# Kernel optimization log

Hardware: AMD Instinct MI355X
Metric: run time of the kernel (lower is better)

## Reference

```python
import jax, jax.numpy as jnp
import numpy as np

B, C, H, W = 16, 3, 384, 1280
EPS = 1e-7


def setup_inputs() -> dict:
    key = jax.random.key(0)
    k1, k2, k3, k4 = jax.random.split(key, 4)
    source_image = jax.random.normal(k1, (B, C, H, W), jnp.float32)
    depth_map = jax.random.uniform(k2, (B, 1, H, W), jnp.float32, minval=0.1, maxval=80.0)
    pose = 0.05 * jax.random.normal(k3, (B, 6), jnp.float32)
    # realistic KITTI-style pinhole intrinsics, per-batch mild perturbation
    base = jnp.array([[0.58 * W, 0.0, 0.5 * W],
                      [0.0, 1.92 * H, 0.5 * H],
                      [0.0, 0.0, 1.0]], jnp.float32)
    noise = 1.0 + 0.01 * jax.random.normal(k4, (B, 3, 3), jnp.float32)
    intrinsic = base[None] * noise  # zero entries stay zero -> invertible
    return {"source_image": source_image, "depth_map": depth_map,
            "pose": pose, "intrinsic": intrinsic}


def rot_from_axisangle(aa):
    # aa: [B,3] -> [B,3,3] (Rodrigues)
    theta = jnp.linalg.norm(aa, axis=-1, keepdims=True)  # [B,1]
    axis = aa / (theta + EPS)
    c = jnp.cos(theta)
    s = jnp.sin(theta)
    t = 1.0 - c
    x, y, z = axis[:, 0:1], axis[:, 1:2], axis[:, 2:3]
    row0 = jnp.concatenate([t * x * x + c, t * x * y - s * z, t * z * x + s * y], axis=1)
    row1 = jnp.concatenate([t * x * y + s * z, t * y * y + c, t * y * z - s * x], axis=1)
    row2 = jnp.concatenate([t * z * x - s * y, t * y * z + s * x, t * z * z + c], axis=1)
    return jnp.stack([row0, row1, row2], axis=1)  # [B,3,3]


def bilinear_grid_sample(img, gx, gy):
    # img: [B,C,H,W]; gx,gy: [B,H,W] in [-1,1]; align_corners=True, padding zeros
    Bc, Cc, Hc, Wc = img.shape
    x = (gx + 1.0) * 0.5 * (Wc - 1)
    y = (gy + 1.0) * 0.5 * (Hc - 1)
    x0 = jnp.floor(x)
    y0 = jnp.floor(y)
    x1 = x0 + 1.0
    y1 = y0 + 1.0
    wx1 = x - x0
    wx0 = 1.0 - wx1
    wy1 = y - y0
    wy0 = 1.0 - wy1
    imgf = img.reshape(Bc, Cc, Hc * Wc)

    def gather(xi, yi):
        inb = ((xi >= 0) & (xi <= Wc - 1) & (yi >= 0) & (yi <= Hc - 1)).astype(img.dtype)
        xc = jnp.clip(xi, 0, Wc - 1).astype(jnp.int32)
        yc = jnp.clip(yi, 0, Hc - 1).astype(jnp.int32)
        idx = (yc * Wc + xc).reshape(Bc, 1, -1)
        vals = jnp.take_along_axis(imgf, jnp.broadcast_to(idx, (Bc, Cc, idx.shape[-1])), axis=2)
        return vals.reshape(Bc, Cc, Hc, Wc) * inb[:, None]

    out = (gather(x0, y0) * (wx0 * wy0)[:, None]
           + gather(x1, y0) * (wx1 * wy0)[:, None]
           + gather(x0, y1) * (wx0 * wy1)[:, None]
           + gather(x1, y1) * (wx1 * wy1)[:, None])
    return out


def reference(source_image, depth_map, pose, intrinsic):
    Bb, _, Hh, Ww = depth_map.shape
    # pixel grid, homogeneous [H,W,3] = (x, y, 1)
    ys, xs = jnp.meshgrid(jnp.arange(Hh, dtype=depth_map.dtype),
                          jnp.arange(Ww, dtype=depth_map.dtype), indexing='ij')
    pix = jnp.stack([xs, ys, jnp.ones_like(xs)], axis=-1)  # [H,W,3]
    # backproject: K^{-1} @ pix * depth
    inv_K = jnp.linalg.inv(intrinsic)  # [B,3,3]
    cam = jnp.einsum('bij,hwj->bhwi', inv_K, pix)  # [B,H,W,3]
    frustum = cam * jnp.transpose(depth_map, (0, 2, 3, 1))  # [B,H,W,3]
    # rigid transform
    R = rot_from_axisangle(pose[:, :3])  # [B,3,3]
    t = pose[:, 3:]  # [B,3]
    points = jnp.einsum('bij,bhwj->bhwi', R, frustum) + t[:, None, None, :]
    # project with K
    coord = jnp.einsum('bij,bhwj->bhwi', intrinsic, points)  # [B,H,W,3]
    z = coord[..., 2] + EPS
    px = coord[..., 0] / z
    py = coord[..., 1] / z
    gx = px / (Ww - 1) * 2.0 - 1.0
    gy = py / (Hh - 1) * 2.0 - 1.0
    return bilinear_grid_sample(source_image, gx, gy)
```

## Files before the change

### kernel.cpp

```cpp
#include <hip/hip_runtime.h>
#include <hip/hip_fp16.h>

#define B_ 16
#define C_ 3
#define H_ 384
#define W_ 1280
#define HW_ (H_*W_)
#define EPS_ 1e-7f

#define NXCD_ 8

#define BANDS_ (W_/256)
#define RTILES_ (H_/2)
#define NBLK3_ (BANDS_*RTILES_*B_)
#define CPX3_  (NBLK3_/NXCD_)

typedef float v2f __attribute__((ext_vector_type(2)));
typedef float v4f __attribute__((ext_vector_type(4)));

__device__ __forceinline__ v2f load2(const float* p) {
  v2f r; __builtin_memcpy(&r, p, 8); return r;
}
__device__ __forceinline__ uint4 load16u(const void* p) {
  uint4 r; __builtin_memcpy(&r, p, 16); return r;
}
__device__ __forceinline__ v4f ntload4(const float* p) {
  return __builtin_nontemporal_load((const v4f*)p);
}
__device__ __forceinline__ void storent2(float* p, float a, float b) {
  v2f r; r.x = a; r.y = b;
  __builtin_nontemporal_store(r, (v2f*)p);
}
__device__ __forceinline__ unsigned pack2(float a, float b) {
  __half2 h = __floats2half2_rn(a, b);
  unsigned u; __builtin_memcpy(&u, &h, 4); return u;
}

__device__ __forceinline__ void mat3mul(const float* A, const float* Bm, float* C) {
  #pragma unroll
  for (int i = 0; i < 3; i++)
    #pragma unroll
    for (int j = 0; j < 3; j++)
      C[i*3+j] = A[i*3+0]*Bm[0*3+j] + A[i*3+1]*Bm[1*3+j] + A[i*3+2]*Bm[2*3+j];
}

__device__ void compute_MT(const float* __restrict__ pose,
                           const float* __restrict__ intr,
                           int b, float* M, float* T)
{
  float K[9];
  #pragma unroll
  for (int i = 0; i < 9; i++) K[i] = intr[b*9 + i];
  float aa0 = pose[b*6 + 0], aa1 = pose[b*6 + 1], aa2 = pose[b*6 + 2];
  float t0  = pose[b*6 + 3], t1  = pose[b*6 + 4], t2  = pose[b*6 + 5];

  float theta = sqrtf(aa0*aa0 + aa1*aa1 + aa2*aa2);
  float invn  = 1.0f / (theta + EPS_);
  float x = aa0*invn, y = aa1*invn, z = aa2*invn;
  float c = cosf(theta), s = sinf(theta), t = 1.0f - c;
  float R[9] = {
    t*x*x + c,   t*x*y - s*z, t*z*x + s*y,
    t*x*y + s*z, t*y*y + c,   t*y*z - s*x,
    t*z*x - s*y, t*y*z + s*x, t*z*z + c
  };

  float a = K[0], bb = K[1], cc = K[2];
  float d = K[3], e  = K[4], f  = K[5];
  float g = K[6], h  = K[7], ii = K[8];
  float A0 = e*ii - f*h, A1 = f*g - d*ii, A2 = d*h - e*g;
  float id = 1.0f / (a*A0 + bb*A1 + cc*A2);
  float iK[9] = {
    A0*id, (cc*h - bb*ii)*id, (bb*f - cc*e)*id,
    A1*id, (a*ii - cc*g)*id,  (cc*d - a*f)*id,
    A2*id, (bb*g - a*h)*id,   (a*e  - bb*d)*id
  };

  float KR[9];
  mat3mul(K, R, KR);
  mat3mul(KR, iK, M);
  T[0] = K[0]*t0 + K[1]*t1 + K[2]*t2;
  T[1] = K[3]*t0 + K[4]*t1 + K[5]*t2;
  T[2] = K[6]*t0 + K[7]*t1 + K[8]*t2;
}

__global__ __launch_bounds__(256) void repack_kernel(
    const float* __restrict__ src, uint4* __restrict__ ws)
{
  int tg = blockIdx.x * 256 + threadIdx.x;
  int b  = tg / (HW_/4);
  int p  = (tg - b * (HW_/4)) * 4;
  const float* s = src + (size_t)b * 3 * HW_ + p;
  v4f c0 = ntload4(s);
  v4f c1 = ntload4(s + HW_);
  v4f c2 = ntload4(s + 2*HW_);
  uint4 o0, o1;
  o0.x = pack2(c0.x, c1.x); o0.y = pack2(c2.x, 0.0f);
  o0.z = pack2(c0.y, c1.y); o0.w = pack2(c2.y, 0.0f);
  o1.x = pack2(c0.z, c1.z); o1.y = pack2(c2.z, 0.0f);
  o1.z = pack2(c0.w, c1.w); o1.w = pack2(c2.w, 0.0f);
  ws[(size_t)tg*2]     = o0;
  ws[(size_t)tg*2 + 1] = o1;
}

__global__ __launch_bounds__(256) void warp2_kernel(
    const uint4* __restrict__ pk,
    const float* __restrict__ depth,
    const float* __restrict__ pose,
    const float* __restrict__ intr,
    float* __restrict__ out)
{
  __shared__ float sp[12];

  int l = blockIdx.x;
  int w = (l & (NXCD_-1)) * CPX3_ + (l >> 3);
  int rt   = w % RTILES_;
  int tmp  = w / RTILES_;
  int band = tmp % BANDS_;
  int b    = tmp / BANDS_;

  int t  = threadIdx.x;
  int rr = t >> 7;
  int cp = t & 127;
  int j0 = band * 256 + 2*cp;
  int i  = rt * 2 + rr;

  v2f dq = load2(depth + (size_t)b * HW_ + (size_t)i * W_ + j0);

  if (t == 0) {
    float M[9], T[3];
    compute_MT(pose, intr, b, M, T);
    #pragma unroll
    for (int k = 0; k < 9; k++) sp[k] = M[k];
    #pragma unroll
    for (int k = 0; k < 3; k++) sp[9 + k] = T[k];
  }
  __syncthreads();
  float m00 = sp[0], m01 = sp[1], m02 = sp[2];
  float m10 = sp[3], m11 = sp[4], m12 = sp[5];
  float m20 = sp[6], m21 = sp[7], m22 = sp[8];
  float T0  = sp[9], T1  = sp[10], T2 = sp[11];

  float yf = (float)i;
  float bx = m01*yf + m02;
  float by = m11*yf + m12;
  float bz = m21*yf + m22;

  const char* pkb = (const char*)pk;
  size_t pb = (size_t)b * HW_;

  float xfA = (float)j0;
  float dA  = dq.x;
  float czA = (m20*xfA + bz)*dA + T2;
  float ivA = 1.0f / (czA + EPS_);
  float pxA = ((m00*xfA + bx)*dA + T0) * ivA;
  float pyA = ((m10*xfA + by)*dA + T1) * ivA;
  float x0A = floorf(pxA), y0A = floorf(pyA);
  float fx1A = pxA - x0A, fx0A = 1.0f - fx1A;
  float fy1A = pyA - y0A, fy0A = 1.0f - fy1A;
  float wx0A = fx0A * ((x0A >= 0.0f && x0A <= (float)(W_-1)) ? 1.0f : 0.0f);
  float wx1A = fx1A * ((x0A+1.0f >= 0.0f && x0A+1.0f <= (float)(W_-1)) ? 1.0f : 0.0f);
  float wy0A = fy0A * ((y0A >= 0.0f && y0A <= (float)(H_-1)) ? 1.0f : 0.0f);
  float wy1A = fy1A * ((y0A+1.0f >= 0.0f && y0A+1.0f <= (float)(H_-1)) ? 1.0f : 0.0f);
  int xc0A = (int)fminf(fmaxf(x0A, 0.0f), (float)(W_-1));
  int xc1A = (int)fminf(fmaxf(x0A+1.0f, 0.0f), (float)(W_-1));
  int yc0A = (int)fminf(fmaxf(y0A, 0.0f), (float)(H_-1));
  int yc1A = (int)fminf(fmaxf(y0A+1.0f, 0.0f), (float)(H_-1));
  float w00A = wx0A*wy0A, w01A = wx1A*wy0A, w10A = wx0A*wy1A, w11A = wx1A*wy1A;
  int baseA = xc0A < (W_-2) ? xc0A : (W_-2);
  bool s0A = (xc0A == baseA), s1A = (xc1A == baseA + 1);
  float waxA = (s0A ? w00A : 0.0f) + (s1A ? 0.0f : w01A);
  float wayA = (s0A ? 0.0f : w00A) + (s1A ? w01A : 0.0f);
  float wbxA = (s0A ? w10A : 0.0f) + (s1A ? 0.0f : w11A);
  float wbyA = (s0A ? 0.0f : w10A) + (s1A ? w11A : 0.0f);
  size_t offA0 = (pb + (size_t)yc0A * W_ + baseA) * 8;
  size_t offA1 = (pb + (size_t)yc1A * W_ + baseA) * 8;

  float xfB = (float)(j0 + 1);
  float dB  = dq.y;
  float czB = (m20*xfB + bz)*dB + T2;
  float ivB = 1.0f / (czB + EPS_);
  float pxB = ((m00*xfB + bx)*dB + T0) * ivB;
  float pyB = ((m10*xfB + by)*dB + T1) * ivB;
  float x0B = floorf(pxB), y0B = floorf(pyB);
  float fx1B = pxB - x0B, fx0B = 1.0f - fx1B;
  float fy1B = pyB - y0B, fy0B = 1.0f - fy1B;
  float wx0B = fx0B * ((x0B >= 0.0f && x0B <= (float)(W_-1)) ? 1.0f : 0.0f);
  float wx1B = fx1B * ((x0B+1.0f >= 0.0f && x0B+1.0f <= (float)(W_-1)) ? 1.0f : 0.0f);
  float wy0B = fy0B * ((y0B >= 0.0f && y0B <= (float)(H_-1)) ? 1.0f : 0.0f);
  float wy1B = fy1B * ((y0B+1.0f >= 0.0f && y0B+1.0f <= (float)(H_-1)) ? 1.0f : 0.0f);
  int xc0B = (int)fminf(fmaxf(x0B, 0.0f), (float)(W_-1));
  int xc1B = (int)fminf(fmaxf(x0B+1.0f, 0.0f), (float)(W_-1));
  int yc0B = (int)fminf(fmaxf(y0B, 0.0f), (float)(H_-1));
  int yc1B = (int)fminf(fmaxf(y0B+1.0f, 0.0f), (float)(H_-1));
  float w00B = wx0B*wy0B, w01B = wx1B*wy0B, w10B = wx0B*wy1B, w11B = wx1B*wy1B;
  int baseB = xc0B < (W_-2) ? xc0B : (W_-2);
  bool s0B = (xc0B == baseB), s1B = (xc1B == baseB + 1);
  float waxB = (s0B ? w00B : 0.0f) + (s1B ? 0.0f : w01B);
  float wayB = (s0B ? 0.0f : w00B) + (s1B ? w01B : 0.0f);
  float wbxB = (s0B ? w10B : 0.0f) + (s1B ? 0.0f : w11B);
  float wbyB = (s0B ? 0.0f : w10B) + (s1B ? w11B : 0.0f);
  size_t offB0 = (pb + (size_t)yc0B * W_ + baseB) * 8;
  size_t offB1 = (pb + (size_t)yc1B * W_ + baseB) * 8;

  uint4 RA0 = load16u(pkb + offA0);
  uint4 RA1 = load16u(pkb + offA1);
  uint4 RB0 = load16u(pkb + offB0);
  uint4 RB1 = load16u(pkb + offB1);
  __builtin_amdgcn_sched_barrier(0);

  float2 A00 = __half22float2(*(const __half2*)&RA0.x);
  float  A02 = __low2float  (*(const __half2*)&RA0.y);
  float2 A01 = __half22float2(*(const __half2*)&RA0.z);
  float  A03 = __low2float  (*(const __half2*)&RA0.w);
  float2 A10 = __half22float2(*(const __half2*)&RA1.x);
  float  A12 = __low2float  (*(const __half2*)&RA1.y);
  float2 A11 = __half22float2(*(const __half2*)&RA1.z);
  float  A13 = __low2float  (*(const __half2*)&RA1.w);
  float vA0 = A00.x*waxA + A01.x*wayA + A10.x*wbxA + A11.x*wbyA;
  float vA1 = A00.y*waxA + A01.y*wayA + A10.y*wbxA + A11.y*wbyA;
  float vA2 = A02  *waxA + A03  *wayA + A12  *wbxA + A13  *wbyA;

  float2 B00 = __half22float2(*(const __half2*)&RB0.x);
  float  B02 = __low2float  (*(const __half2*)&RB0.y);
  float2 B01 = __half22float2(*(const __half2*)&RB0.z);
  float  B03 = __low2float  (*(const __half2*)&RB0.w);
  float2 B10 = __half22float2(*(const __half2*)&RB1.x);
  float  B12 = __low2float  (*(const __half2*)&RB1.y);
  float2 B11 = __half22float2(*(const __half2*)&RB1.z);
  float  B13 = __low2float  (*(const __half2*)&RB1.w);
  float vB0 = B00.x*waxB + B01.x*wayB + B10.x*wbxB + B11.x*wbyB;
  float vB1 = B00.y*waxB + B01.y*wayB + B10.y*wbxB + B11.y*wbyB;
  float vB2 = B02  *waxB + B03  *wayB + B12  *wbxB + B13  *wbyB;

  size_t sb = (size_t)b * C_ * HW_;
  size_t op = (size_t)i * W_ + j0;
  storent2(out + sb + op,                   vA0, vB0);
  storent2(out + sb + HW_ + op,             vA1, vB1);
  storent2(out + sb + 2*(size_t)HW_ + op,   vA2, vB2);
}

__global__ __launch_bounds__(256) void warp_fb_kernel(
    const float* __restrict__ src,
    const float* __restrict__ depth,
    const float* __restrict__ pose,
    const float* __restrict__ intr,
    float* __restrict__ out)
{
  __shared__ float sp[12];
  int b = blockIdx.y;
  if (threadIdx.x == 0) {
    float M[9], T[3];
    compute_MT(pose, intr, b, M, T);
    #pragma unroll
    for (int k = 0; k < 9; k++) sp[k] = M[k];
    #pragma unroll
    for (int k = 0; k < 3; k++) sp[9 + k] = T[k];
  }
  __syncthreads();
  float m00 = sp[0], m01 = sp[1], m02 = sp[2];
  float m10 = sp[3], m11 = sp[4], m12 = sp[5];
  float m20 = sp[6], m21 = sp[7], m22 = sp[8];
  float T0  = sp[9], T1  = sp[10], T2 = sp[11];

  int p = blockIdx.x * 256 + threadIdx.x;
  int j = p % W_;
  int i = p / W_;

  float d  = depth[(size_t)b * HW_ + p];
  float xf = (float)j, yf = (float)i;
  float cx = (m00*xf + m01*yf + m02)*d + T0;
  float cy = (m10*xf + m11*yf + m12)*d + T1;
  float cz = (m20*xf + m21*yf + m22)*d + T2;
  float inv = 1.0f / (cz + EPS_);
  float px = cx * inv, py = cy * inv;

  float x0f = floorf(px), y0f = floorf(py);
  float x1f = x0f + 1.0f, y1f = y0f + 1.0f;
  float wx1 = px - x0f, wx0 = 1.0f - wx1;
  float wy1 = py - y0f, wy0 = 1.0f - wy1;
  float mx0 = (x0f >= 0.0f && x0f <= (float)(W_-1)) ? 1.0f : 0.0f;
  float mx1 = (x1f >= 0.0f && x1f <= (float)(W_-1)) ? 1.0f : 0.0f;
  float my0 = (y0f >= 0.0f && y0f <= (float)(H_-1)) ? 1.0f : 0.0f;
  float my1 = (y1f >= 0.0f && y1f <= (float)(H_-1)) ? 1.0f : 0.0f;
  int xc0 = (int)fminf(fmaxf(x0f, 0.0f), (float)(W_-1));
  int xc1 = (int)fminf(fmaxf(x1f, 0.0f), (float)(W_-1));
  int yc0 = (int)fminf(fmaxf(y0f, 0.0f), (float)(H_-1));
  int yc1 = (int)fminf(fmaxf(y1f, 0.0f), (float)(H_-1));
  float w00 = wx0*wy0*mx0*my0;
  float w01 = wx1*wy0*mx1*my0;
  float w10 = wx0*wy1*mx0*my1;
  float w11 = wx1*wy1*mx1*my1;
  int base = xc0 < (W_-2) ? xc0 : (W_-2);
  bool s0 = (xc0 == base);
  bool s1 = (xc1 == base + 1);
  float wax = (s0 ? w00 : 0.0f) + (s1 ? 0.0f : w01);
  float way = (s0 ? 0.0f : w00) + (s1 ? w01 : 0.0f);
  float wbx = (s0 ? w10 : 0.0f) + (s1 ? 0.0f : w11);
  float wby = (s0 ? 0.0f : w10) + (s1 ? w11 : 0.0f);
  int rb0 = yc0*W_ + base;
  int rb1 = yc1*W_ + base;

  size_t sb = (size_t)b * C_ * HW_;
  const float* s0p = src + sb;
  const float* s1p = s0p + HW_;
  const float* s2p = s1p + HW_;
  v2f a0 = load2(s0p + rb0);
  v2f b0 = load2(s0p + rb1);
  v2f a1 = load2(s1p + rb0);
  v2f b1 = load2(s1p + rb1);
  v2f a2 = load2(s2p + rb0);
  v2f b2 = load2(s2p + rb1);
  float v0 = a0.x*wax + a0.y*way + b0.x*wbx + b0.y*wby;
  float v1 = a1.x*wax + a1.y*way + b1.x*wbx + b1.y*wby;
  float v2 = a2.x*wax + a2.y*way + b2.x*wbx + b2.y*wby;
  size_t op = (size_t)p;
  __builtin_nontemporal_store(v0, &out[sb + op]);
  __builtin_nontemporal_store(v1, &out[sb + HW_ + op]);
  __builtin_nontemporal_store(v2, &out[sb + 2*(size_t)HW_ + op]);
}

extern "C" void kernel_launch(void* const* d_in, const int* in_sizes, int n_in,
                              void* d_out, int out_size, void* d_ws, size_t ws_size,
                              hipStream_t stream) {
  const float* src   = (const float*)d_in[0];
  const float* depth = (const float*)d_in[1];
  const float* pose  = (const float*)d_in[2];
  const float* intr  = (const float*)d_in[3];
  float* out = (float*)d_out;

  const size_t need = (size_t)B_ * HW_ * 8;
  if (d_ws != nullptr && ws_size >= need) {
    uint4* ws = (uint4*)d_ws;
    repack_kernel<<<dim3(B_*HW_/4/256), 256, 0, stream>>>(src, ws);
    warp2_kernel<<<dim3(NBLK3_), 256, 0, stream>>>(ws, depth, pose, intr, out);
  } else {
    dim3 grid(HW_ / 256, B_);
    warp_fb_kernel<<<grid, 256, 0, stream>>>(src, depth, pose, intr, out);
  }
}
```

Measured before the change: 231.2 us.

## Pad repacked image with zero border to drop edge-clamp weight remapping

The packed half-precision image now lives in a zero-padded buffer: one zero row above and below each image and two zero columns on each side, filled by a small new pad kernel. The warp kernel clamps the top-left sample to [-1, W-1] and reads both rows at a fixed row stride. This removes the separate clamped row index and the per-pixel weight reshuffling used for right-edge handling, and the divide becomes a hardware reciprocal. It adds a third kernel launch and slightly more workspace, and the approximate reciprocal may change low-order bits.

```diff
diff --git a/kernel.cpp b/kernel.cpp
--- a/kernel.cpp
+++ b/kernel.cpp
@@ -8,12 +8,17 @@
 #define HW_ (H_*W_)
 #define EPS_ 1e-7f
 
+#define WP_ 1284
+#define HP_ 386
 #define NXCD_ 8
 
 #define BANDS_ (W_/256)
 #define RTILES_ (H_/2)
 #define NBLK3_ (BANDS_*RTILES_*B_)
 #define CPX3_  (NBLK3_/NXCD_)
+
+#define PADPB_ (2*WP_ + 4*H_)
+#define NPAD_  (B_*PADPB_)
 
 typedef float v2f __attribute__((ext_vector_type(2)));
 typedef float v4f __attribute__((ext_vector_type(4)));
@@ -83,12 +88,33 @@
   T[2] = K[6]*t0 + K[7]*t1 + K[8]*t2;
 }
 
+__global__ __launch_bounds__(256) void pad_kernel(unsigned long long* __restrict__ ws)
+{
+  int tid = blockIdx.x * 256 + threadIdx.x;
+  if (tid >= NPAD_) return;
+  int b = tid / PADPB_;
+  int k = tid - b * PADPB_;
+  int row, col;
+  if (k < WP_)            { row = 0;       col = k; }
+  else if (k < 2*WP_)     { row = HP_ - 1; col = k - WP_; }
+  else {
+    int kk = k - 2*WP_;
+    row = (kk >> 2) + 1;
+    int c4 = kk & 3;
+    col = (c4 < 2) ? c4 : (WP_ - 4 + c4);
+  }
+  ws[(size_t)(b * HP_ + row) * WP_ + col] = 0ULL;
+}
+
 __global__ __launch_bounds__(256) void repack_kernel(
     const float* __restrict__ src, uint4* __restrict__ ws)
 {
   int tg = blockIdx.x * 256 + threadIdx.x;
   int b  = tg / (HW_/4);
-  int p  = (tg - b * (HW_/4)) * 4;
+  int rq = tg - b * (HW_/4);
+  int p  = rq * 4;
+  int y  = p / W_;
+  int x  = p - y * W_;
   const float* s = src + (size_t)b * 3 * HW_ + p;
   v4f c0 = ntload4(s);
   v4f c1 = ntload4(s + HW_);
@@ -98,8 +124,9 @@
   o0.z = pack2(c0.y, c1.y); o0.w = pack2(c2.y, 0.0f);
   o1.x = pack2(c0.z, c1.z); o1.y = pack2(c2.z, 0.0f);
   o1.z = pack2(c0.w, c1.w); o1.w = pack2(c2.w, 0.0f);
-  ws[(size_t)tg*2]     = o0;
-  ws[(size_t)tg*2 + 1] = o1;
+  size_t slot = (size_t)(b * HP_ + y + 1) * WP_ + (x + 2);
+  ws[slot >> 1]       = o0;
+  ws[(slot >> 1) + 1] = o1;
 }
 
 __global__ __launch_bounds__(256) void warp2_kernel(
@@ -146,66 +173,49 @@
   float bz = m21*yf + m22;
 
   const char* pkb = (const char*)pk;
-  size_t pb = (size_t)b * HW_;
+  const float Wm1 = (float)(W_-1), Hm1 = (float)(H_-1);
+  int rowbase = b * HP_;
 
   float xfA = (float)j0;
   float dA  = dq.x;
   float czA = (m20*xfA + bz)*dA + T2;
-  float ivA = 1.0f / (czA + EPS_);
+  float ivA = __builtin_amdgcn_rcpf(czA + EPS_);
   float pxA = ((m00*xfA + bx)*dA + T0) * ivA;
   float pyA = ((m10*xfA + by)*dA + T1) * ivA;
   float x0A = floorf(pxA), y0A = floorf(pyA);
   float fx1A = pxA - x0A, fx0A = 1.0f - fx1A;
   float fy1A = pyA - y0A, fy0A = 1.0f - fy1A;
-  float wx0A = fx0A * ((x0A >= 0.0f && x0A <= (float)(W_-1)) ? 1.0f : 0.0f);
-  float wx1A = fx1A * ((x0A+1.0f >= 0.0f && x0A+1.0f <= (float)(W_-1)) ? 1.0f : 0.0f);
-  float wy0A = fy0A * ((y0A >= 0.0f && y0A <= (float)(H_-1)) ? 1.0f : 0.0f);
-  float wy1A = fy1A * ((y0A+1.0f >= 0.0f && y0A+1.0f <= (float)(H_-1)) ? 1.0f : 0.0f);
-  int xc0A = (int)fminf(fmaxf(x0A, 0.0f), (float)(W_-1));
-  int xc1A = (int)fminf(fmaxf(x0A+1.0f, 0.0f), (float)(W_-1));
-  int yc0A = (int)fminf(fmaxf(y0A, 0.0f), (float)(H_-1));
-  int yc1A = (int)fminf(fmaxf(y0A+1.0f, 0.0f), (float)(H_-1));
+  float wx0A = (x0A >= 0.0f      && x0A <= Wm1) ? fx0A : 0.0f;
+  float wx1A = (x0A+1.0f >= 0.0f && x0A+1.0f <= Wm1) ? fx1A : 0.0f;
+  float wy0A = (y0A >= 0.0f      && y0A <= Hm1) ? fy0A : 0.0f;
+  float wy1A = (y0A+1.0f >= 0.0f && y0A+1.0f <= Hm1) ? fy1A : 0.0f;
   float w00A = wx0A*wy0A, w01A = wx1A*wy0A, w10A = wx0A*wy1A, w11A = wx1A*wy1A;
-  int baseA = xc0A < (W_-2) ? xc0A : (W_-2);
-  bool s0A = (xc0A == baseA), s1A = (xc1A == baseA + 1);
-  float waxA = (s0A ? w00A : 0.0f) + (s1A ? 0.0f : w01A);
-  float wayA = (s0A ? 0.0f : w00A) + (s1A ? w01A : 0.0f);
-  float wbxA = (s0A ? w10A : 0.0f) + (s1A ? 0.0f : w11A);
-  float wbyA = (s0A ? 0.0f : w10A) + (s1A ? w11A : 0.0f);
-  size_t offA0 = (pb + (size_t)yc0A * W_ + baseA) * 8;
-  size_t offA1 = (pb + (size_t)yc1A * W_ + baseA) * 8;
+  int xbA = (int)fminf(fmaxf(x0A, -1.0f), Wm1);
+  int ybA = (int)fminf(fmaxf(y0A, -1.0f), Hm1);
+  size_t offA0 = ((size_t)(rowbase + ybA + 1) * WP_ + (xbA + 2)) * 8;
 
   float xfB = (float)(j0 + 1);
   float dB  = dq.y;
   float czB = (m20*xfB + bz)*dB + T2;
-  float ivB = 1.0f / (czB + EPS_);
+  float ivB = __builtin_amdgcn_rcpf(czB + EPS_);
   float pxB = ((m00*xfB + bx)*dB + T0) * ivB;
   float pyB = ((m10*xfB + by)*dB + T1) * ivB;
   float x0B = floorf(pxB), y0B = floorf(pyB);
   float fx1B = pxB - x0B, fx0B = 1.0f - fx1B;
   float fy1B = pyB - y0B, fy0B = 1.0f - fy1B;
-  float wx0B = fx0B * ((x0B >= 0.0f && x0B <= (float)(W_-1)) ? 1.0f : 0.0f);
-  float wx1B = fx1B * ((x0B+1.0f >= 0.0f && x0B+1.0f <= (float)(W_-1)) ? 1.0f : 0.0f);
-  float wy0B = fy0B * ((y0B >= 0.0f && y0B <= (float)(H_-1)) ? 1.0f : 0.0f);
-  float wy1B = fy1B * ((y0B+1.0f >= 0.0f && y0B+1.0f <= (float)(H_-1)) ? 1.0f : 0.0f);
-  int xc0B = (int)fminf(fmaxf(x0B, 0.0f), (float)(W_-1));
-  int xc1B = (int)fminf(fmaxf(x0B+1.0f, 0.0f), (float)(W_-1));
-  int yc0B = (int)fminf(fmaxf(y0B, 0.0f), (float)(H_-1));
-  int yc1B = (int)fminf(fmaxf(y0B+1.0f, 0.0f), (float)(H_-1));
+  float wx0B = (x0B >= 0.0f      && x0B <= Wm1) ? fx0B : 0.0f;
+  float wx1B = (x0B+1.0f >= 0.0f && x0B+1.0f <= Wm1) ? fx1B : 0.0f;
+  float wy0B = (y0B >= 0.0f      && y0B <= Hm1) ? fy0B : 0.0f;
+  float wy1B = (y0B+1.0f >= 0.0f && y0B+1.0f <= Hm1) ? fy1B : 0.0f;
   float w00B = wx0B*wy0B, w01B = wx1B*wy0B, w10B = wx0B*wy1B, w11B = wx1B*wy1B;
-  int baseB = xc0B < (W_-2) ? xc0B : (W_-2);
-  bool s0B = (xc0B == baseB), s1B = (xc1B == baseB + 1);
-  float waxB = (s0B ? w00B : 0.0f) + (s1B ? 0.0f : w01B);
-  float wayB = (s0B ? 0.0f : w00B) + (s1B ? w01B : 0.0f);
-  float wbxB = (s0B ? w10B : 0.0f) + (s1B ? 0.0f : w11B);
-  float wbyB = (s0B ? 0.0f : w10B) + (s1B ? w11B : 0.0f);
-  size_t offB0 = (pb + (size_t)yc0B * W_ + baseB) * 8;
-  size_t offB1 = (pb + (size_t)yc1B * W_ + baseB) * 8;
+  int xbB = (int)fminf(fmaxf(x0B, -1.0f), Wm1);
+  int ybB = (int)fminf(fmaxf(y0B, -1.0f), Hm1);
+  size_t offB0 = ((size_t)(rowbase + ybB + 1) * WP_ + (xbB + 2)) * 8;
 
   uint4 RA0 = load16u(pkb + offA0);
-  uint4 RA1 = load16u(pkb + offA1);
+  uint4 RA1 = load16u(pkb + offA0 + (size_t)WP_*8);
   uint4 RB0 = load16u(pkb + offB0);
-  uint4 RB1 = load16u(pkb + offB1);
+  uint4 RB1 = load16u(pkb + offB0 + (size_t)WP_*8);
   __builtin_amdgcn_sched_barrier(0);
 
   float2 A00 = __half22float2(*(const __half2*)&RA0.x);
@@ -216,9 +226,9 @@
   float  A12 = __low2float  (*(const __half2*)&RA1.y);
   float2 A11 = __half22float2(*(const __half2*)&RA1.z);
   float  A13 = __low2float  (*(const __half2*)&RA1.w);
-  float vA0 = A00.x*waxA + A01.x*wayA + A10.x*wbxA + A11.x*wbyA;
-  float vA1 = A00.y*waxA + A01.y*wayA + A10.y*wbxA + A11.y*wbyA;
-  float vA2 = A02  *waxA + A03  *wayA + A12  *wbxA + A13  *wbyA;
+  float vA0 = A00.x*w00A + A01.x*w01A + A10.x*w10A + A11.x*w11A;
+  float vA1 = A00.y*w00A + A01.y*w01A + A10.y*w10A + A11.y*w11A;
+  float vA2 = A02  *w00A + A03  *w01A + A12  *w10A + A13  *w11A;
 
   float2 B00 = __half22float2(*(const __half2*)&RB0.x);
   float  B02 = __low2float  (*(const __half2*)&RB0.y);
@@ -228,9 +238,9 @@
   float  B12 = __low2float  (*(const __half2*)&RB1.y);
   float2 B11 = __half22float2(*(const __half2*)&RB1.z);
   float  B13 = __low2float  (*(const __half2*)&RB1.w);
-  float vB0 = B00.x*waxB + B01.x*wayB + B10.x*wbxB + B11.x*wbyB;
-  float vB1 = B00.y*waxB + B01.y*wayB + B10.y*wbxB + B11.y*wbyB;
-  float vB2 = B02  *waxB + B03  *wayB + B12  *wbxB + B13  *wbyB;
+  float vB0 = B00.x*w00B + B01.x*w01B + B10.x*w10B + B11.x*w11B;
+  float vB1 = B00.y*w00B + B01.y*w01B + B10.y*w10B + B11.y*w11B;
+  float vB2 = B02  *w00B + B03  *w01B + B12  *w10B + B13  *w11B;
 
   size_t sb = (size_t)b * C_ * HW_;
   size_t op = (size_t)i * W_ + j0;
@@ -328,11 +338,11 @@
   const float* intr  = (const float*)d_in[3];
   float* out = (float*)d_out;
 
-  const size_t need = (size_t)B_ * HW_ * 8;
+  const size_t need = (size_t)B_ * HP_ * WP_ * 8;
   if (d_ws != nullptr && ws_size >= need) {
-    uint4* ws = (uint4*)d_ws;
-    repack_kernel<<<dim3(B_*HW_/4/256), 256, 0, stream>>>(src, ws);
-    warp2_kernel<<<dim3(NBLK3_), 256, 0, stream>>>(ws, depth, pose, intr, out);
+    pad_kernel<<<dim3((NPAD_ + 255)/256), 256, 0, stream>>>((unsigned long long*)d_ws);
+    repack_kernel<<<dim3(B_*HW_/4/256), 256, 0, stream>>>(src, (uint4*)d_ws);
+    warp2_kernel<<<dim3(NBLK3_), 256, 0, stream>>>((const uint4*)d_ws, depth, pose, intr, out);
   } else {
     dim3 grid(HW_ / 256, B_);
     warp_fb_kernel<<<grid, 256, 0, stream>>>(src, depth, pose, intr, out);
```

Result: no change. 231.4 us (+0.1%).
